# Optimization experiments

Measured on AMD Instinct MI355X. Metric: run time of the kernel, lower is better.

## Reference

```python
import jax, jax.numpy as jnp
import numpy as np

B, L, D_IN, D_MODEL, D_STATE, D_DISCR, KER = 2, 1024, 512, 1024, 16, 64, 4


def setup_inputs() -> dict:
    ks = jax.random.split(jax.random.key(0), 9)
    s = 0.02
    return {
        "seq": jax.random.normal(ks[0], (B, L, D_IN), jnp.float32),
        "W_in": jax.random.normal(ks[1], (2 * D_MODEL, D_IN), jnp.float32) * s,
        "W_out": jax.random.normal(ks[2], (D_IN, D_MODEL), jnp.float32) * s,
        "W_B": jax.random.normal(ks[3], (D_STATE, D_MODEL), jnp.float32) * s,
        "W_C": jax.random.normal(ks[4], (D_STATE, D_MODEL), jnp.float32) * s,
        "W_D1": jax.random.normal(ks[5], (D_DISCR, D_MODEL), jnp.float32) * s,
        "W_D2": jax.random.normal(ks[6], (D_MODEL, D_DISCR), jnp.float32) * s,
        "conv_w": jax.random.normal(ks[7], (D_MODEL, 1, KER), jnp.float32) * 0.1,
        "conv_b": jax.random.normal(ks[8], (D_MODEL,), jnp.float32) * 0.01,
        "A": jnp.tile(jnp.arange(1, D_STATE + 1, dtype=jnp.float32), (D_MODEL, 1)),
        "D": jnp.ones((D_MODEL,), jnp.float32),
    }


def _causal_depthwise_conv(x, w, b):
    # x: [B, L, D] -> torch Conv1d(groups=D, padding=KER-1) truncated to first L outputs
    x = jnp.swapaxes(x, 1, 2)  # [B, D, L]
    y = jax.lax.conv_general_dilated(
        x, w, window_strides=(1,), padding=[(KER - 1, 0)],
        dimension_numbers=("NCH", "OIH", "NCH"), feature_group_count=D_MODEL)
    y = y + b[None, :, None]
    return jnp.swapaxes(y, 1, 2)  # [B, L, D]


def _ssm(x, W_B, W_C, W_D1, W_D2, A, D):
    # x: [B, L, D]
    exp_negA = jnp.exp(-A)                                  # [D, S]
    Bm = jnp.einsum("bld,sd->bls", x, W_B)                  # [B, L, S]
    Cm = jnp.einsum("bld,sd->bls", x, W_C)                  # [B, L, S]
    delta = jax.nn.softplus(D + jnp.einsum("ble,de->bld", jnp.einsum("bld,ed->ble", x, W_D1), W_D2))  # [B, L, D]
    A_bar = exp_negA[None, None] * delta[..., None]         # [B, L, D, S]
    X = Bm[:, :, None, :] * delta[..., None] * x[..., None]  # [B, L, D, S]

    def comb(c1, c2):
        a1, x1 = c1
        a2, x2 = c2
        return a1 * a2, a2 * x1 + x2

    _, h = jax.lax.associative_scan(comb, (A_bar, X), axis=1)  # h: [B, L, D, S]
    y = jnp.einsum("blds,bls->bld", h, Cm)
    return y + D * x


def reference(seq, W_in, W_out, W_B, W_C, W_D1, W_D2, conv_w, conv_b, A, D):
    ab = jnp.einsum("bli,oi->blo", seq, W_in)   # [B, L, 2*D_MODEL]
    a, b = ab[..., :D_MODEL], ab[..., D_MODEL:]
    a = jax.nn.silu(_causal_depthwise_conv(a, conv_w, conv_b))
    a = _ssm(a, W_B, W_C, W_D1, W_D2, A, D)
    out = a * jax.nn.silu(b)
    return jnp.einsum("bld,od->blo", out, W_out)  # [B, L, D_IN]
```

## Files before the change

### kernel.cpp

```cpp
#include <hip/hip_runtime.h>
#include <hip/hip_bf16.h>

typedef short short8 __attribute__((ext_vector_type(8)));
typedef short short4v __attribute__((ext_vector_type(4)));
typedef float float4v __attribute__((ext_vector_type(4)));

#define B_   2
#define L_   1024
#define DIN  512
#define DM   1024
#define DS   16
#define DD   64
#define KER_ 4
#define NROW (B_*L_)

#define SD   4
#define SC   128
#define SLC  8

__device__ __forceinline__ float silu_f(float v){ return v / (1.f + expf(-v)); }

__device__ __forceinline__ short2 f2bf2(float a, float b) {
  __hip_bfloat162 h = __float22bfloat162_rn(float2{a, b});
  union { __hip_bfloat162 h; short2 s; } u; u.h = h; return u.s;
}
__device__ __forceinline__ short f2bf1(float a) {
  __hip_bfloat16 h = __float2bfloat16(a);
  union { __hip_bfloat16 h; short s; } u; u.h = h; return u.s;
}
__device__ __forceinline__ short8 pack8(const float4& x0, const float4& x1) {
  short2 s0 = f2bf2(x0.x, x0.y), s1 = f2bf2(x0.z, x0.w);
  short2 s2 = f2bf2(x1.x, x1.y), s3 = f2bf2(x1.z, x1.w);
  return short8{ s0.x, s0.y, s1.x, s1.y, s2.x, s2.y, s3.x, s3.y };
}
__device__ __forceinline__ float bf2f(short s) {
  union { unsigned u; float f; } v; v.u = ((unsigned)(unsigned short)s) << 16; return v.f;
}

__global__ __launch_bounds__(256)
void gemm1_k(const float* __restrict__ seq, const float* __restrict__ Win,
             __hip_bfloat16* __restrict__ ab, float* __restrict__ pall) {
  __shared__ short As[64 * 40];
  __shared__ short Bs[64 * 40];
  const int tid  = threadIdx.x;
  {
    int zi = (blockIdx.y * 32 + blockIdx.x) * 256 + tid;
    if (zi < NROW * 96) pall[zi] = 0.f;
  }
  const int lane = tid & 63;
  const int wave = tid >> 6;
  const int r16  = lane & 15;
  const int quad = lane >> 4;
  const int m0 = blockIdx.y * 64;
  const int n0 = blockIdx.x * 64;
  const int wm = wave & 1, wn = wave >> 1;
  float4v acc[2][2];
#pragma unroll
  for (int i = 0; i < 2; i++)
#pragma unroll
    for (int j = 0; j < 2; j++) acc[i][j] = (float4v){0.f, 0.f, 0.f, 0.f};
  float4 pf0[2], pf1[2];
  auto ldu = [&](int j, int k0) {
    int u = tid + j * 256;
    const float4* p;
    if (u < 256) { int row = u >> 2, q = u & 3;
      p = (const float4*)(seq + (size_t)(m0 + row) * DIN + k0 + q * 8);
    } else { int v = u - 256; int row = v >> 2, q = v & 3;
      p = (const float4*)(Win + (size_t)(n0 + row) * DIN + k0 + q * 8);
    }
    pf0[j] = p[0]; pf1[j] = p[1];
  };
  auto stu = [&](int j) {
    int u = tid + j * 256;
    short8 s = pack8(pf0[j], pf1[j]);
    if (u < 256) { int row = u >> 2, q = u & 3; *(short8*)&As[row * 40 + q * 8] = s; }
    else { int v = u - 256; int row = v >> 2, q = v & 3; *(short8*)&Bs[row * 40 + q * 8] = s; }
  };
  ldu(0, 0); ldu(1, 0);
  for (int k0 = 0; k0 < DIN; k0 += 32) {
    stu(0); stu(1);
    __syncthreads();
    if (k0 + 32 < DIN) { ldu(0, k0 + 32); ldu(1, k0 + 32); }
    short8 afr[2], bfr[2];
#pragma unroll
    for (int mi = 0; mi < 2; mi++)
      afr[mi] = *(const short8*)&As[(wm * 32 + mi * 16 + r16) * 40 + quad * 8];
#pragma unroll
    for (int ni = 0; ni < 2; ni++)
      bfr[ni] = *(const short8*)&Bs[(wn * 32 + ni * 16 + r16) * 40 + quad * 8];
#pragma unroll
    for (int mi = 0; mi < 2; mi++)
#pragma unroll
      for (int ni = 0; ni < 2; ni++)
        acc[mi][ni] = __builtin_amdgcn_mfma_f32_16x16x32_bf16(afr[mi], bfr[ni], acc[mi][ni], 0, 0, 0);
    __syncthreads();
  }
#pragma unroll
  for (int mi = 0; mi < 2; mi++)
#pragma unroll
    for (int ni = 0; ni < 2; ni++) {
      int gn = n0 + wn * 32 + ni * 16 + r16;
#pragma unroll
      for (int r = 0; r < 4; r++) {
        int gm = m0 + wm * 32 + mi * 16 + quad * 4 + r;
        ab[(size_t)gm * (2 * DM) + gn] = __float2bfloat16(acc[mi][ni][r]);
      }
    }
}

__global__ __launch_bounds__(256)
void convproj_k(const __hip_bfloat16* __restrict__ ab, const float* __restrict__ cw,
                const float* __restrict__ cb, const float* __restrict__ WB,
                const float* __restrict__ WC, const float* __restrict__ WD1,
                float* __restrict__ xt, short* __restrict__ gt,
                float* __restrict__ pall) {
  __shared__ char smraw[12800];
  const int blk = blockIdx.x;
  const int tid = threadIdx.x;

  if (blk < 1024) {
    short* tile = (short*)smraw;
    const int n0 = (blk & 31) * 64;
    const int d0 = (blk >> 5) * 64;
    const int l0 = n0 & (L_ - 1);
    for (int u = tid; u < 67 * 8; u += 256) {
      int r = u >> 3, c8 = u & 7;
      int l = l0 - 3 + r;
      short8 v = short8{0, 0, 0, 0, 0, 0, 0, 0};
      if (l >= 0 && r < 67)
        v = *(const short8*)(ab + (size_t)(n0 - l0 + l) * (2 * DM) + d0 + c8 * 8);
      *(short8*)&tile[r * 74 + c8 * 8] = v;
    }
    __syncthreads();
    const int i  = tid & 63;
    const int dl = tid >> 6;
    if (d0 < DM) {
#pragma unroll 4
      for (int p = 0; p < 16; p++) {
        int dc = p * 4 + dl;
        int d  = d0 + dc;
        float4 w = *(const float4*)(cw + d * 4);
        float a = cb[d];
        a += bf2f(tile[(i + 0) * 74 + dc]) * w.x;
        a += bf2f(tile[(i + 1) * 74 + dc]) * w.y;
        a += bf2f(tile[(i + 2) * 74 + dc]) * w.z;
        a += bf2f(tile[(i + 3) * 74 + dc]) * w.w;
        xt[(size_t)d * NROW + n0 + i] = silu_f(a);
      }
    } else {
#pragma unroll 4
      for (int p = 0; p < 16; p++) {
        int dc = p * 4 + dl;
        gt[(size_t)(d0 - DM + dc) * NROW + n0 + i] = tile[(i + 3) * 74 + dc];
      }
    }
    return;
  }

  short* As = (short*)smraw;
  short* Bs = As + 64 * 40;
  const int b2   = blk - 1024;
  const int lane = tid & 63;
  const int wave = tid >> 6;
  const int r16  = lane & 15;
  const int quad = lane >> 4;
  const int m0   = (b2 & 31) * 64;
  const int kbeg = (b2 >> 5) * 128;
  float4v acc[6];
#pragma unroll
  for (int i = 0; i < 6; i++) acc[i] = (float4v){0.f, 0.f, 0.f, 0.f};

  short8 ta[KER_];
  float4 pf0[2], pf1[2];
  const int arow = tid >> 2, aq = tid & 3;
  const int an = m0 + arow, al = an & (L_ - 1), abq = an >> 10;

  auto ldu_a = [&](int k0) {
#pragma unroll
    for (int t = 0; t < KER_; t++) {
      int ll = al - (KER_ - 1) + t;
      if (ll >= 0)
        ta[t] = *(const short8*)(ab + (size_t)(abq * L_ + ll) * (2 * DM) + k0 + aq * 8);
      else
        ta[t] = short8{0, 0, 0, 0, 0, 0, 0, 0};
    }
  };
  auto stu_a = [&](int k0) {
    float r8[8];
#pragma unroll
    for (int e = 0; e < 8; e++) {
      int d = k0 + aq * 8 + e;
      float4 w = *(const float4*)(cw + d * 4);
      float a = cb[d];
      a += bf2f(ta[0][e]) * w.x;
      a += bf2f(ta[1][e]) * w.y;
      a += bf2f(ta[2][e]) * w.z;
      a += bf2f(ta[3][e]) * w.w;
      r8[e] = silu_f(a);
    }
    *(short8*)&As[arow * 40 + aq * 8] =
        pack8(float4{r8[0], r8[1], r8[2], r8[3]}, float4{r8[4], r8[5], r8[6], r8[7]});
  };
  auto ldu_b = [&](int j, int k0) {
    int u = tid + j * 256;
    if (u >= 640) return;
    int v = u - 256, row = v >> 2, q = v & 3;
    const float* bp = (row < 16) ? (WB + (size_t)row * DM)
                    : (row < 32) ? (WC + (size_t)(row - 16) * DM)
                                 : (WD1 + (size_t)(row - 32) * DM);
    const float4* p = (const float4*)(bp + k0 + q * 8);
    pf0[j - 1] = p[0]; pf1[j - 1] = p[1];
  };
  auto stu_b = [&](int j) {
    int u = tid + j * 256;
    if (u >= 640) return;
    int v = u - 256, row = v >> 2, q = v & 3;
    *(short8*)&Bs[row * 40 + q * 8] = pack8(pf0[j - 1], pf1[j - 1]);
  };

  ldu_a(kbeg); ldu_b(1, kbeg); ldu_b(2, kbeg);
  for (int k0 = kbeg; k0 < kbeg + 128; k0 += 32) {
    stu_a(k0); stu_b(1); stu_b(2);
    __syncthreads();
    if (k0 + 32 < kbeg + 128) { ldu_a(k0 + 32); ldu_b(1, k0 + 32); ldu_b(2, k0 + 32); }
    short8 afr = *(const short8*)&As[(wave * 16 + r16) * 40 + quad * 8];
#pragma unroll
    for (int ni = 0; ni < 6; ni++) {
      short8 bfr = *(const short8*)&Bs[(ni * 16 + r16) * 40 + quad * 8];
      acc[ni] = __builtin_amdgcn_mfma_f32_16x16x32_bf16(afr, bfr, acc[ni], 0, 0, 0);
    }
    __syncthreads();
  }
#pragma unroll
  for (int ni = 0; ni < 6; ni++) {
    int gn = ni * 16 + r16;
#pragma unroll
    for (int r = 0; r < 4; r++) {
      int gm = m0 + wave * 16 + quad * 4 + r;
      atomicAdd(&pall[(size_t)gm * 96 + gn], acc[ni][r]);
    }
  }
}

__global__ __launch_bounds__(256)
void delta_k(const float* __restrict__ t1, const float* __restrict__ WD2,
             const float* __restrict__ Dv, float* __restrict__ dltT) {
  __shared__ short As[64 * 40];
  __shared__ short Bs[64 * 40];
  const int tid  = threadIdx.x;
  const int lane = tid & 63;
  const int wave = tid >> 6;
  const int r16  = lane & 15;
  const int quad = lane >> 4;
  const int m0 = blockIdx.y * 64;
  const int n0 = blockIdx.x * 64;
  const int wm = wave & 1, wn = wave >> 1;
  float4v acc[2][2];
#pragma unroll
  for (int i = 0; i < 2; i++)
#pragma unroll
    for (int j = 0; j < 2; j++) acc[i][j] = (float4v){0.f, 0.f, 0.f, 0.f};
  float4 pf0[2], pf1[2];
  auto ldu = [&](int j, int k0) {
    int u = tid + j * 256;
    const float4* p;
    if (u < 256) { int row = u >> 2, q = u & 3;
      p = (const float4*)(t1 + (size_t)(m0 + row) * 96 + k0 + q * 8);
    } else { int v = u - 256; int row = v >> 2, q = v & 3;
      p = (const float4*)(WD2 + (size_t)(n0 + row) * DD + k0 + q * 8);
    }
    pf0[j] = p[0]; pf1[j] = p[1];
  };
  auto stu = [&](int j) {
    int u = tid + j * 256;
    short8 s = pack8(pf0[j], pf1[j]);
    if (u < 256) { int row = u >> 2, q = u & 3; *(short8*)&As[row * 40 + q * 8] = s; }
    else { int v = u - 256; int row = v >> 2, q = v & 3; *(short8*)&Bs[row * 40 + q * 8] = s; }
  };
  ldu(0, 0); ldu(1, 0);
  for (int k0 = 0; k0 < DD; k0 += 32) {
    stu(0); stu(1);
    __syncthreads();
    if (k0 + 32 < DD) { ldu(0, k0 + 32); ldu(1, k0 + 32); }
    short8 afr[2], bfr[2];
#pragma unroll
    for (int mi = 0; mi < 2; mi++)
      afr[mi] = *(const short8*)&As[(wm * 32 + mi * 16 + r16) * 40 + quad * 8];
#pragma unroll
    for (int ni = 0; ni < 2; ni++)
      bfr[ni] = *(const short8*)&Bs[(wn * 32 + ni * 16 + r16) * 40 + quad * 8];
#pragma unroll
    for (int mi = 0; mi < 2; mi++)
#pragma unroll
      for (int ni = 0; ni < 2; ni++)
        acc[mi][ni] = __builtin_amdgcn_mfma_f32_16x16x32_bf16(afr[mi], bfr[ni], acc[mi][ni], 0, 0, 0);
    __syncthreads();
  }
#pragma unroll
  for (int mi = 0; mi < 2; mi++)
#pragma unroll
    for (int ni = 0; ni < 2; ni++) {
      int gn = n0 + wn * 32 + ni * 16 + r16;
      float dvn = Dv[gn];
#pragma unroll
      for (int r = 0; r < 4; r++) {
        int gm = m0 + wm * 32 + mi * 16 + quad * 4 + r;
        float v = acc[mi][ni][r] + dvn;
        v = fmaxf(v, 0.f) + log1pf(expf(-fabsf(v)));
        dltT[(size_t)gn * NROW + gm] = v;
      }
    }
}

__global__ __launch_bounds__(512, 4)
void scan_fused_k(const float* __restrict__ xt, const float* __restrict__ dltT,
                  const float* __restrict__ pall, const float* __restrict__ A,
                  const float* __restrict__ Dv, const short* __restrict__ gt,
                  short* __restrict__ soutb) {
  __shared__ float Pl[DS * SD][SC + 1];
  __shared__ float Hl[DS * SD][SC + 1];
  const int blk = blockIdx.x;
  const int b   = blk >> 8;
  const int d0  = (blk & 255) * SD;
  const int dd  = threadIdx.x & (SD - 1);
  const int c   = threadIdx.x >> 2;
  const int d   = d0 + dd;

  float e[DS], esl[DS];
#pragma unroll
  for (int s = 0; s < DS; s++) {
    float a = A[d * DS + s];
    e[s]   = expf(-a);
    esl[s] = expf(-(float)SLC * a);
  }
  const int nbase = b * L_ + c * SLC;
  const float* xrow = xt   + (size_t)d * NROW;
  const float* drow = dltT + (size_t)d * NROW;
  const short* grow = gt   + (size_t)d * NROW;

  float h[DS];
#pragma unroll
  for (int s = 0; s < DS; s++) h[s] = 0.f;
  float pdl = 1.f;
#pragma unroll
  for (int q = 0; q < SLC / 4; q++) {
    const int n = nbase + q * 4;
    float4 x4 = *(const float4*)(xrow + n);
    float4 d4 = *(const float4*)(drow + n);
    float4 bq[4][4];
#pragma unroll
    for (int t = 0; t < 4; t++) {
      const float4* pp = (const float4*)(pall + (size_t)(n + t) * 96);
      bq[t][0] = pp[0]; bq[t][1] = pp[1]; bq[t][2] = pp[2]; bq[t][3] = pp[3];
    }
#pragma unroll
    for (int t = 0; t < 4; t++) {
      float dl = (&d4.x)[t], xv = (&x4.x)[t];
      float dx = dl * xv;
      pdl *= dl;
      float bmv[DS] = { bq[t][0].x, bq[t][0].y, bq[t][0].z, bq[t][0].w,
                        bq[t][1].x, bq[t][1].y, bq[t][1].z, bq[t][1].w,
                        bq[t][2].x, bq[t][2].y, bq[t][2].z, bq[t][2].w,
                        bq[t][3].x, bq[t][3].y, bq[t][3].z, bq[t][3].w };
#pragma unroll
      for (int s = 0; s < DS; s++)
        h[s] = (e[s] * dl) * h[s] + bmv[s] * dx;
    }
  }
#pragma unroll
  for (int s = 0; s < DS; s++) {
    Pl[s * SD + dd][c] = esl[s] * pdl;
    Hl[s * SD + dd][c] = h[s];
  }
  __syncthreads();

  if (threadIdx.x < DS * SD) {
    float* Prow = &Pl[threadIdx.x][0];
    float* Hrow = &Hl[threadIdx.x][0];
    float H = 0.f;
    for (int c2 = 0; c2 < SC; c2++) {
      float pp = Prow[c2];
      float hh = Hrow[c2];
      Prow[c2] = H;
      H = pp * H + hh;
    }
  }
  __syncthreads();

#pragma unroll
  for (int s = 0; s < DS; s++) h[s] = Pl[s * SD + dd][c];
  float Dd = Dv[d];
#pragma unroll
  for (int q = 0; q < SLC / 4; q++) {
    const int n = nbase + q * 4;
    float4 x4 = *(const float4*)(xrow + n);
    float4 d4 = *(const float4*)(drow + n);
    short4v g4 = *(const short4v*)(grow + n);
    float4 bq[4][4], cq[4][4];
#pragma unroll
    for (int t = 0; t < 4; t++) {
      const float4* pp = (const float4*)(pall + (size_t)(n + t) * 96);
      bq[t][0] = pp[0]; bq[t][1] = pp[1]; bq[t][2] = pp[2]; bq[t][3] = pp[3];
      cq[t][0] = pp[4]; cq[t][1] = pp[5]; cq[t][2] = pp[6]; cq[t][3] = pp[7];
    }
#pragma unroll
    for (int t = 0; t < 4; t++) {
      float dl = (&d4.x)[t], xv = (&x4.x)[t];
      float dx = dl * xv;
      float bmv[DS] = { bq[t][0].x, bq[t][0].y, bq[t][0].z, bq[t][0].w,
                        bq[t][1].x, bq[t][1].y, bq[t][1].z, bq[t][1].w,
                        bq[t][2].x, bq[t][2].y, bq[t][2].z, bq[t][2].w,
                        bq[t][3].x, bq[t][3].y, bq[t][3].z, bq[t][3].w };
      float cmv[DS] = { cq[t][0].x, cq[t][0].y, cq[t][0].z, cq[t][0].w,
                        cq[t][1].x, cq[t][1].y, cq[t][1].z, cq[t][1].w,
                        cq[t][2].x, cq[t][2].y, cq[t][2].z, cq[t][2].w,
                        cq[t][3].x, cq[t][3].y, cq[t][3].z, cq[t][3].w };
      float y = 0.f;
#pragma unroll
      for (int s = 0; s < DS; s++) {
        h[s] = (e[s] * dl) * h[s] + bmv[s] * dx;
        y += h[s] * cmv[s];
      }
      y += Dd * xv;
      float g = bf2f(g4[t]);
      soutb[(size_t)(n + t) * DM + d] = f2bf1(y * silu_f(g));
    }
  }
}

__global__ __launch_bounds__(256)
void gemm2_k(const short* __restrict__ soutb, const float* __restrict__ Wout,
             float* __restrict__ out) {
  __shared__ short As[64 * 40];
  __shared__ short Bs[32 * 40];
  const int tid  = threadIdx.x;
  const int lane = tid & 63;
  const int wave = tid >> 6;
  const int r16  = lane & 15;
  const int quad = lane >> 4;
  const int m0 = blockIdx.y * 64;
  const int n0 = blockIdx.x * 32;
  const int wm = wave & 1, wn = wave >> 1;
  float4v acc[2];
  acc[0] = (float4v){0.f, 0.f, 0.f, 0.f};
  acc[1] = (float4v){0.f, 0.f, 0.f, 0.f};
  short8 pa;
  float4 pf0, pf1;
  auto ldu = [&](int k0) {
    {
      int row = tid >> 2, q = tid & 3;
      pa = *(const short8*)(soutb + (size_t)(m0 + row) * DM + k0 + q * 8);
    }
    if (tid < 128) {
      int row = tid >> 2, q = tid & 3;
      const float4* p = (const float4*)(Wout + (size_t)(n0 + row) * DM + k0 + q * 8);
      pf0 = p[0]; pf1 = p[1];
    }
  };
  auto stu = [&]() {
    { int row = tid >> 2, q = tid & 3; *(short8*)&As[row * 40 + q * 8] = pa; }
    if (tid < 128) { int row = tid >> 2, q = tid & 3; *(short8*)&Bs[row * 40 + q * 8] = pack8(pf0, pf1); }
  };
  ldu(0);
  for (int k0 = 0; k0 < DM; k0 += 32) {
    stu();
    __syncthreads();
    if (k0 + 32 < DM) ldu(k0 + 32);
    short8 afr[2], bfr;
    afr[0] = *(const short8*)&As[(wm * 32 + r16) * 40 + quad * 8];
    afr[1] = *(const short8*)&As[(wm * 32 + 16 + r16) * 40 + quad * 8];
    bfr    = *(const short8*)&Bs[(wn * 16 + r16) * 40 + quad * 8];
    acc[0] = __builtin_amdgcn_mfma_f32_16x16x32_bf16(afr[0], bfr, acc[0], 0, 0, 0);
    acc[1] = __builtin_amdgcn_mfma_f32_16x16x32_bf16(afr[1], bfr, acc[1], 0, 0, 0);
    __syncthreads();
  }
#pragma unroll
  for (int mi = 0; mi < 2; mi++)
#pragma unroll
    for (int r = 0; r < 4; r++)
      out[(size_t)(m0 + wm * 32 + mi * 16 + quad * 4 + r) * DIN + n0 + wn * 16 + r16] = acc[mi][r];
}

extern "C" void kernel_launch(void* const* d_in, const int* in_sizes, int n_in,
                              void* d_out, int out_size, void* d_ws, size_t ws_size,
                              hipStream_t stream) {
  const float* seq  = (const float*)d_in[0];
  const float* Win  = (const float*)d_in[1];
  const float* Wout = (const float*)d_in[2];
  const float* WB   = (const float*)d_in[3];
  const float* WC   = (const float*)d_in[4];
  const float* WD1  = (const float*)d_in[5];
  const float* WD2  = (const float*)d_in[6];
  const float* cw   = (const float*)d_in[7];
  const float* cb   = (const float*)d_in[8];
  const float* A    = (const float*)d_in[9];
  const float* Dv   = (const float*)d_in[10];
  float* out = (float*)d_out;

  float* ws = (float*)d_ws;
  __hip_bfloat16* ab = (__hip_bfloat16*)ws;
  float* xt   = ws   + 2097152;
  short* gt   = (short*)(xt + 2097152);
  float* dltT = (float*)(gt + 2097152);
  float* pall = dltT + 2097152;
  short* soutb = (short*)(pall + 196608);
  float* t1   = pall + 32;

  gemm1_k<<<dim3(32, 32), 256, 0, stream>>>(seq, Win, ab, pall);
  convproj_k<<<1280, 256, 0, stream>>>(ab, cw, cb, WB, WC, WD1, xt, gt, pall);
  delta_k<<<dim3(16, 32), 256, 0, stream>>>(t1, WD2, Dv, dltT);
  scan_fused_k<<<B_ * (DM / SD), 512, 0, stream>>>(xt, dltT, pall, A, Dv, gt, soutb);
  gemm2_k<<<dim3(16, 32), 256, 0, stream>>>(soutb, Wout, out);
}
```

Measured before the change: 162.5 us.

## Fuse delta projection into scan kernel and parallelize chunk-carry scan

Removes the separate delta_k GEMM kernel. Each scan thread now computes its own 8 delta values from the low-rank t1 projection and the WD2 row, in FP32, followed by softplus. This avoids a kernel launch plus writing and re-reading the 8MB transposed delta buffer. It also replaces the serial 128-step per-state carry scan, run by 64 threads, with a two-level scan: 8 segments per state run in parallel over all 512 threads, then a short 8-step serial pass. The cost is redundant dot-product work, since each t1 row is read by every d-thread, and more registers in a kernel already bounded at 512 threads × 4 blocks.

Result: slower. 296.3 us (+82.3%).

```diff
diff --git a/kernel.cpp b/kernel.cpp
--- a/kernel.cpp
+++ b/kernel.cpp
@@ -17,6 +17,7 @@
 #define SD   4
 #define SC   128
 #define SLC  8
+#define NSEG 8
 
 __device__ __forceinline__ float silu_f(float v){ return v / (1.f + expf(-v)); }
 
@@ -242,83 +243,15 @@
   }
 }
 
-__global__ __launch_bounds__(256)
-void delta_k(const float* __restrict__ t1, const float* __restrict__ WD2,
-             const float* __restrict__ Dv, float* __restrict__ dltT) {
-  __shared__ short As[64 * 40];
-  __shared__ short Bs[64 * 40];
-  const int tid  = threadIdx.x;
-  const int lane = tid & 63;
-  const int wave = tid >> 6;
-  const int r16  = lane & 15;
-  const int quad = lane >> 4;
-  const int m0 = blockIdx.y * 64;
-  const int n0 = blockIdx.x * 64;
-  const int wm = wave & 1, wn = wave >> 1;
-  float4v acc[2][2];
-#pragma unroll
-  for (int i = 0; i < 2; i++)
-#pragma unroll
-    for (int j = 0; j < 2; j++) acc[i][j] = (float4v){0.f, 0.f, 0.f, 0.f};
-  float4 pf0[2], pf1[2];
-  auto ldu = [&](int j, int k0) {
-    int u = tid + j * 256;
-    const float4* p;
-    if (u < 256) { int row = u >> 2, q = u & 3;
-      p = (const float4*)(t1 + (size_t)(m0 + row) * 96 + k0 + q * 8);
-    } else { int v = u - 256; int row = v >> 2, q = v & 3;
-      p = (const float4*)(WD2 + (size_t)(n0 + row) * DD + k0 + q * 8);
-    }
-    pf0[j] = p[0]; pf1[j] = p[1];
-  };
-  auto stu = [&](int j) {
-    int u = tid + j * 256;
-    short8 s = pack8(pf0[j], pf1[j]);
-    if (u < 256) { int row = u >> 2, q = u & 3; *(short8*)&As[row * 40 + q * 8] = s; }
-    else { int v = u - 256; int row = v >> 2, q = v & 3; *(short8*)&Bs[row * 40 + q * 8] = s; }
-  };
-  ldu(0, 0); ldu(1, 0);
-  for (int k0 = 0; k0 < DD; k0 += 32) {
-    stu(0); stu(1);
-    __syncthreads();
-    if (k0 + 32 < DD) { ldu(0, k0 + 32); ldu(1, k0 + 32); }
-    short8 afr[2], bfr[2];
-#pragma unroll
-    for (int mi = 0; mi < 2; mi++)
-      afr[mi] = *(const short8*)&As[(wm * 32 + mi * 16 + r16) * 40 + quad * 8];
-#pragma unroll
-    for (int ni = 0; ni < 2; ni++)
-      bfr[ni] = *(const short8*)&Bs[(wn * 32 + ni * 16 + r16) * 40 + quad * 8];
-#pragma unroll
-    for (int mi = 0; mi < 2; mi++)
-#pragma unroll
-      for (int ni = 0; ni < 2; ni++)
-        acc[mi][ni] = __builtin_amdgcn_mfma_f32_16x16x32_bf16(afr[mi], bfr[ni], acc[mi][ni], 0, 0, 0);
-    __syncthreads();
-  }
-#pragma unroll
-  for (int mi = 0; mi < 2; mi++)
-#pragma unroll
-    for (int ni = 0; ni < 2; ni++) {
-      int gn = n0 + wn * 32 + ni * 16 + r16;
-      float dvn = Dv[gn];
-#pragma unroll
-      for (int r = 0; r < 4; r++) {
-        int gm = m0 + wm * 32 + mi * 16 + quad * 4 + r;
-        float v = acc[mi][ni][r] + dvn;
-        v = fmaxf(v, 0.f) + log1pf(expf(-fabsf(v)));
-        dltT[(size_t)gn * NROW + gm] = v;
-      }
-    }
-}
-
 __global__ __launch_bounds__(512, 4)
-void scan_fused_k(const float* __restrict__ xt, const float* __restrict__ dltT,
-                  const float* __restrict__ pall, const float* __restrict__ A,
-                  const float* __restrict__ Dv, const short* __restrict__ gt,
+void scan_fused_k(const float* __restrict__ xt, const float* __restrict__ pall,
+                  const float* __restrict__ A, const float* __restrict__ Dv,
+                  const float* __restrict__ WD2, const short* __restrict__ gt,
                   short* __restrict__ soutb) {
   __shared__ float Pl[DS * SD][SC + 1];
   __shared__ float Hl[DS * SD][SC + 1];
+  __shared__ float Ps[DS * SD][NSEG + 1];
+  __shared__ float Hs[DS * SD][NSEG + 1];
   const int blk = blockIdx.x;
   const int b   = blk >> 8;
   const int d0  = (blk & 255) * SD;
@@ -326,17 +259,45 @@
   const int c   = threadIdx.x >> 2;
   const int d   = d0 + dd;
 
-  float e[DS], esl[DS];
-#pragma unroll
-  for (int s = 0; s < DS; s++) {
-    float a = A[d * DS + s];
-    e[s]   = expf(-a);
-    esl[s] = expf(-(float)SLC * a);
-  }
+  float e[DS];
+#pragma unroll
+  for (int s = 0; s < DS; s++) e[s] = expf(-A[d * DS + s]);
+
   const int nbase = b * L_ + c * SLC;
-  const float* xrow = xt   + (size_t)d * NROW;
-  const float* drow = dltT + (size_t)d * NROW;
-  const short* grow = gt   + (size_t)d * NROW;
+  const float* xrow = xt + (size_t)d * NROW;
+  const short* grow = gt + (size_t)d * NROW;
+  const float Dd = Dv[d];
+
+  float dlt[SLC];
+#pragma unroll
+  for (int t = 0; t < SLC; t++) dlt[t] = Dd;
+  {
+    const float* wrow = WD2 + (size_t)d * DD;
+#pragma unroll
+    for (int kq = 0; kq < 4; kq++) {
+      float4 w0 = *(const float4*)(wrow + kq * 16 + 0);
+      float4 w1 = *(const float4*)(wrow + kq * 16 + 4);
+      float4 w2 = *(const float4*)(wrow + kq * 16 + 8);
+      float4 w3 = *(const float4*)(wrow + kq * 16 + 12);
+#pragma unroll
+      for (int t = 0; t < SLC; t++) {
+        const float* trow = pall + (size_t)(nbase + t) * 96 + 32 + kq * 16;
+        float4 a0 = *(const float4*)(trow + 0);
+        float4 a1 = *(const float4*)(trow + 4);
+        float4 a2 = *(const float4*)(trow + 8);
+        float4 a3 = *(const float4*)(trow + 12);
+        dlt[t] += a0.x * w0.x + a0.y * w0.y + a0.z * w0.z + a0.w * w0.w
+                + a1.x * w1.x + a1.y * w1.y + a1.z * w1.z + a1.w * w1.w
+                + a2.x * w2.x + a2.y * w2.y + a2.z * w2.z + a2.w * w2.w
+                + a3.x * w3.x + a3.y * w3.y + a3.z * w3.z + a3.w * w3.w;
+      }
+    }
+#pragma unroll
+    for (int t = 0; t < SLC; t++) {
+      float v = dlt[t];
+      dlt[t] = fmaxf(v, 0.f) + log1pf(expf(-fabsf(v)));
+    }
+  }
 
   float h[DS];
 #pragma unroll
@@ -346,7 +307,6 @@
   for (int q = 0; q < SLC / 4; q++) {
     const int n = nbase + q * 4;
     float4 x4 = *(const float4*)(xrow + n);
-    float4 d4 = *(const float4*)(drow + n);
     float4 bq[4][4];
 #pragma unroll
     for (int t = 0; t < 4; t++) {
@@ -355,7 +315,7 @@
     }
 #pragma unroll
     for (int t = 0; t < 4; t++) {
-      float dl = (&d4.x)[t], xv = (&x4.x)[t];
+      float dl = dlt[q * 4 + t], xv = (&x4.x)[t];
       float dx = dl * xv;
       pdl *= dl;
       float bmv[DS] = { bq[t][0].x, bq[t][0].y, bq[t][0].z, bq[t][0].w,
@@ -369,32 +329,55 @@
   }
 #pragma unroll
   for (int s = 0; s < DS; s++) {
-    Pl[s * SD + dd][c] = esl[s] * pdl;
+    float e2 = e[s] * e[s], e4 = e2 * e2, e8 = e4 * e4;
+    Pl[s * SD + dd][c] = e8 * pdl;
     Hl[s * SD + dd][c] = h[s];
   }
   __syncthreads();
 
+  {
+    const int seg = threadIdx.x >> 6;
+    const int cmb = threadIdx.x & 63;
+    float* Prow = &Pl[cmb][0];
+    float* Hrow = &Hl[cmb][0];
+    float Pa = 1.f, Ha = 0.f;
+#pragma unroll
+    for (int i = 0; i < SC / NSEG; i++) {
+      int c2 = seg * (SC / NSEG) + i;
+      float p = Prow[c2], hh = Hrow[c2];
+      Prow[c2] = Pa;
+      Hrow[c2] = Ha;
+      Ha = p * Ha + hh;
+      Pa *= p;
+    }
+    Ps[cmb][seg] = Pa;
+    Hs[cmb][seg] = Ha;
+  }
+  __syncthreads();
+
   if (threadIdx.x < DS * SD) {
-    float* Prow = &Pl[threadIdx.x][0];
-    float* Hrow = &Hl[threadIdx.x][0];
+    float* Pr = &Ps[threadIdx.x][0];
+    float* Hr = &Hs[threadIdx.x][0];
     float H = 0.f;
-    for (int c2 = 0; c2 < SC; c2++) {
-      float pp = Prow[c2];
-      float hh = Hrow[c2];
-      Prow[c2] = H;
-      H = pp * H + hh;
+#pragma unroll
+    for (int g = 0; g < NSEG; g++) {
+      float p = Pr[g], hh = Hr[g];
+      Hr[g] = H;
+      H = p * H + hh;
     }
   }
   __syncthreads();
 
-#pragma unroll
-  for (int s = 0; s < DS; s++) h[s] = Pl[s * SD + dd][c];
-  float Dd = Dv[d];
+  {
+    const int g = c >> 4;
+#pragma unroll
+    for (int s = 0; s < DS; s++)
+      h[s] = Pl[s * SD + dd][c] * Hs[s * SD + dd][g] + Hl[s * SD + dd][c];
+  }
 #pragma unroll
   for (int q = 0; q < SLC / 4; q++) {
     const int n = nbase + q * 4;
     float4 x4 = *(const float4*)(xrow + n);
-    float4 d4 = *(const float4*)(drow + n);
     short4v g4 = *(const short4v*)(grow + n);
     float4 bq[4][4], cq[4][4];
 #pragma unroll
@@ -405,7 +388,7 @@
     }
 #pragma unroll
     for (int t = 0; t < 4; t++) {
-      float dl = (&d4.x)[t], xv = (&x4.x)[t];
+      float dl = dlt[q * 4 + t], xv = (&x4.x)[t];
       float dx = dl * xv;
       float bmv[DS] = { bq[t][0].x, bq[t][0].y, bq[t][0].z, bq[t][0].w,
                         bq[t][1].x, bq[t][1].y, bq[t][1].z, bq[t][1].w,
@@ -422,8 +405,8 @@
         y += h[s] * cmv[s];
       }
       y += Dd * xv;
-      float g = bf2f(g4[t]);
-      soutb[(size_t)(n + t) * DM + d] = f2bf1(y * silu_f(g));
+      float gg = bf2f(g4[t]);
+      soutb[(size_t)(n + t) * DM + d] = f2bf1(y * silu_f(gg));
     }
   }
 }
@@ -501,14 +484,11 @@
   __hip_bfloat16* ab = (__hip_bfloat16*)ws;
   float* xt   = ws   + 2097152;
   short* gt   = (short*)(xt + 2097152);
-  float* dltT = (float*)(gt + 2097152);
-  float* pall = dltT + 2097152;
+  float* pall = (float*)(gt + 2097152);
   short* soutb = (short*)(pall + 196608);
-  float* t1   = pall + 32;
 
   gemm1_k<<<dim3(32, 32), 256, 0, stream>>>(seq, Win, ab, pall);
   convproj_k<<<1280, 256, 0, stream>>>(ab, cw, cb, WB, WC, WD1, xt, gt, pall);
-  delta_k<<<dim3(16, 32), 256, 0, stream>>>(t1, WD2, Dv, dltT);
-  scan_fused_k<<<B_ * (DM / SD), 512, 0, stream>>>(xt, dltT, pall, A, Dv, gt, soutb);
+  scan_fused_k<<<B_ * (DM / SD), 512, 0, stream>>>(xt, pall, A, Dv, WD2, gt, soutb);
   gemm2_k<<<dim3(16, 32), 256, 0, stream>>>(soutb, Wout, out);
 }
```

## Parallelize inter-chunk scan carry with two-level segmented scan across all threads

Applied to the files above, without the earlier changes.

Replaces the serial 128-step carry scan run by 64 threads with a two-level scan. All 512 threads each scan a 16-chunk segment, then 64 threads scan the 8 segment totals, and each chunk's initial state is rebuilt as P*carry+H. This targets the long serial phase where most of the block sits idle, at the cost of an extra barrier and more shared memory. Launch bounds drop to 2 blocks per SM, and esl is now computed by repeated squaring instead of expf, which frees registers.

Result: no change. 162.1 us (-0.3%).

```diff
diff --git a/kernel.cpp b/kernel.cpp
--- a/kernel.cpp
+++ b/kernel.cpp
@@ -17,6 +17,7 @@
 #define SD   4
 #define SC   128
 #define SLC  8
+#define NSEG 8
 
 __device__ __forceinline__ float silu_f(float v){ return v / (1.f + expf(-v)); }
 
@@ -312,13 +313,15 @@
     }
 }
 
-__global__ __launch_bounds__(512, 4)
+__global__ __launch_bounds__(512, 2)
 void scan_fused_k(const float* __restrict__ xt, const float* __restrict__ dltT,
                   const float* __restrict__ pall, const float* __restrict__ A,
                   const float* __restrict__ Dv, const short* __restrict__ gt,
                   short* __restrict__ soutb) {
   __shared__ float Pl[DS * SD][SC + 1];
   __shared__ float Hl[DS * SD][SC + 1];
+  __shared__ float Ps[DS * SD][NSEG + 1];
+  __shared__ float Hs[DS * SD][NSEG + 1];
   const int blk = blockIdx.x;
   const int b   = blk >> 8;
   const int d0  = (blk & 255) * SD;
@@ -326,13 +329,10 @@
   const int c   = threadIdx.x >> 2;
   const int d   = d0 + dd;
 
-  float e[DS], esl[DS];
-#pragma unroll
-  for (int s = 0; s < DS; s++) {
-    float a = A[d * DS + s];
-    e[s]   = expf(-a);
-    esl[s] = expf(-(float)SLC * a);
-  }
+  float e[DS];
+#pragma unroll
+  for (int s = 0; s < DS; s++) e[s] = expf(-A[d * DS + s]);
+
   const int nbase = b * L_ + c * SLC;
   const float* xrow = xt   + (size_t)d * NROW;
   const float* drow = dltT + (size_t)d * NROW;
@@ -369,27 +369,52 @@
   }
 #pragma unroll
   for (int s = 0; s < DS; s++) {
-    Pl[s * SD + dd][c] = esl[s] * pdl;
-    Hl[s * SD + dd][c] = h[s];
+    float e2 = e[s] * e[s], e4 = e2 * e2, e8 = e4 * e4;
+    Pl[dd * DS + s][c] = e8 * pdl;
+    Hl[dd * DS + s][c] = h[s];
   }
   __syncthreads();
 
+  {
+    const int seg = threadIdx.x >> 6;
+    const int cmb = threadIdx.x & 63;
+    float* Prow = &Pl[cmb][0];
+    float* Hrow = &Hl[cmb][0];
+    float Pa = 1.f, Ha = 0.f;
+#pragma unroll
+    for (int i = 0; i < SC / NSEG; i++) {
+      int c2 = seg * (SC / NSEG) + i;
+      float p = Prow[c2], hh = Hrow[c2];
+      Prow[c2] = Pa;
+      Hrow[c2] = Ha;
+      Ha = p * Ha + hh;
+      Pa *= p;
+    }
+    Ps[cmb][seg] = Pa;
+    Hs[cmb][seg] = Ha;
+  }
+  __syncthreads();
+
   if (threadIdx.x < DS * SD) {
-    float* Prow = &Pl[threadIdx.x][0];
-    float* Hrow = &Hl[threadIdx.x][0];
+    float* Pr = &Ps[threadIdx.x][0];
+    float* Hr = &Hs[threadIdx.x][0];
     float H = 0.f;
-    for (int c2 = 0; c2 < SC; c2++) {
-      float pp = Prow[c2];
-      float hh = Hrow[c2];
-      Prow[c2] = H;
-      H = pp * H + hh;
+#pragma unroll
+    for (int g = 0; g < NSEG; g++) {
+      float p = Pr[g], hh = Hr[g];
+      Hr[g] = H;
+      H = p * H + hh;
     }
   }
   __syncthreads();
 
-#pragma unroll
-  for (int s = 0; s < DS; s++) h[s] = Pl[s * SD + dd][c];
-  float Dd = Dv[d];
+  {
+    const int g = c >> 4;
+#pragma unroll
+    for (int s = 0; s < DS; s++)
+      h[s] = Pl[dd * DS + s][c] * Hs[dd * DS + s][g] + Hl[dd * DS + s][c];
+  }
+  const float Dd = Dv[d];
 #pragma unroll
   for (int q = 0; q < SLC / 4; q++) {
     const int n = nbase + q * 4;
@@ -422,8 +447,8 @@
         y += h[s] * cmv[s];
       }
       y += Dd * xv;
-      float g = bf2f(g4[t]);
-      soutb[(size_t)(n + t) * DM + d] = f2bf1(y * silu_f(g));
+      float gg = bf2f(g4[t]);
+      soutb[(size_t)(n + t) * DM + d] = f2bf1(y * silu_f(gg));
     }
   }
 }
```
